# Performance work log

Hardware: AMD Instinct MI355X
Metric: run time of the kernel (lower is better)

The kernel has to match this reference:

```python
import jax, jax.numpy as jnp
import numpy as np

B, T, E, H, L = 16, 512, 768, 12, 100
D = E // H
LN_EPS = 1e-12
NEG = -1e9


def setup_inputs() -> dict:
    key = jax.random.key(0)
    ks = jax.random.split(key, 12)
    s = 1.0 / np.sqrt(E)
    inp = {
        "last_hidden_states": jax.random.normal(ks[0], (B, T, E), jnp.float32),
        "att_mask": jnp.ones((B, T), jnp.float32),
        "type_emb": jax.random.normal(ks[1], (L, E), jnp.float32),
        # learned params
        "tp": jax.random.normal(ks[2], (E,), jnp.float32),
        "Wq": jax.random.normal(ks[3], (E, E), jnp.float32) * s,
        "bq": jnp.zeros((E,), jnp.float32),
        "Wk": jax.random.normal(ks[4], (E, E), jnp.float32) * s,
        "bk": jnp.zeros((E,), jnp.float32),
        "Wv": jax.random.normal(ks[5], (E, E), jnp.float32) * s,
        "bv": jnp.zeros((E,), jnp.float32),
        "Wo": jax.random.normal(ks[6], (E, E), jnp.float32) * s,
        "bo": jnp.zeros((E,), jnp.float32),
        "ln_g": jnp.ones((E,), jnp.float32),
        "ln_b": jnp.zeros((E,), jnp.float32),
    }
    return inp


def _layer_norm(x, g, b):
    mu = x.mean(-1, keepdims=True)
    var = ((x - mu) ** 2).mean(-1, keepdims=True)
    return (x - mu) * jax.lax.rsqrt(var + LN_EPS) * g + b


def reference(last_hidden_states, att_mask, type_emb, tp,
              Wq, bq, Wk, bk, Wv, bv, Wo, bo, ln_g, ln_b):
    b, t, e = last_hidden_states.shape
    # --- label cross-attention (no head split, no scaling) ---
    scores = jnp.einsum('bte,le->btl', last_hidden_states, type_emb)      # [b,t,l]
    att = jax.nn.softmax(scores, axis=-1)
    first_label_emb = jnp.einsum('btl,le->bte', att, type_emb)            # [b,t,e]

    h_truth = last_hidden_states + first_label_emb
    h_unknown = last_hidden_states + tp                                   # broadcast tp over [b,t]

    # --- two-stream masked self-attention: Q from unknown, K/V from truth,
    #     each position masked from attending to its own truth state ---
    q = (h_unknown @ Wq + bq).reshape(b, t, H, D)
    k = (h_truth @ Wk + bk).reshape(b, t, H, D)
    v = (h_truth @ Wv + bv).reshape(b, t, H, D)
    logits = jnp.einsum('bqhd,bkhd->bhqk', q, k) / np.sqrt(D).astype(np.float32)
    pad_bias = (1.0 - att_mask)[:, None, None, :] * NEG                   # [b,1,1,t]
    diag_bias = jnp.eye(t, dtype=logits.dtype)[None, None] * NEG          # [1,1,t,t]
    probs = jax.nn.softmax(logits + pad_bias + diag_bias, axis=-1)
    ctx = jnp.einsum('bhqk,bkhd->bqhd', probs, v).reshape(b, t, e)
    attn_out = ctx @ Wo + bo
    twice_hidden = _layer_norm(attn_out + h_unknown, ln_g, ln_b)

    out = twice_hidden + last_hidden_states + first_label_emb
    return out, scores
```

## Files before the change

kernel.cpp:

```cpp
#include <hip/hip_runtime.h>

typedef unsigned char u8;
typedef unsigned short u16;
typedef u16 u16x4 __attribute__((ext_vector_type(4)));
typedef u16 u16x8 __attribute__((ext_vector_type(8)));
typedef __bf16 bf16x8 __attribute__((ext_vector_type(8)));
typedef float f32x2 __attribute__((ext_vector_type(2)));
typedef float f32x4 __attribute__((ext_vector_type(4)));
typedef long longx2 __attribute__((ext_vector_type(2)));

#define BB 16
#define TT 512
#define EE 768
#define HH 12
#define DD 64
#define LL 100
#define BT (BB*TT)
#define BTE ((size_t)BT*EE)
#define LOG2E 1.44269504f
#define QSCALE (0.125f*LOG2E)
#define FIXMAX 44.0f

__device__ __forceinline__ float bf2f(u16 u){
  union { float f; unsigned int i; } v; v.i = ((unsigned int)u) << 16; return v.f;
}
__device__ __forceinline__ u16 f2bf(float f){
  __bf16 h = (__bf16)f;
  union { __bf16 h; u16 u; } v; v.h = h; return v.u;
}
__device__ __forceinline__ u16 pk_fp8(float a, float b){
  return (u16)(__builtin_amdgcn_cvt_pk_fp8_f32(a, b, 0, false) & 0xffff);
}
__device__ __forceinline__ u8 f2fp8(float a){
  return (u8)(__builtin_amdgcn_cvt_pk_fp8_f32(a, 0.f, 0, false) & 0xff);
}

__device__ __forceinline__ void gload16(const void* g, void* l){
  __builtin_amdgcn_global_load_lds(
      (const __attribute__((address_space(1))) void*)g,
      (__attribute__((address_space(3))) void*)l, 16, 0, 0);
}

__global__ __launch_bounds__(256,1) void prep_all_kernel(
    const float* __restrict__ Wq, const float* __restrict__ Wk,
    const float* __restrict__ Wv, const float* __restrict__ Wo,
    u8* __restrict__ WT8,
    const float* __restrict__ TE, u16* __restrict__ TEb, u16* __restrict__ TEt,
    const float* __restrict__ mask, float* __restrict__ MBg)
{
  __shared__ float tile[64][65];
  int bx = blockIdx.x;
  int tid = threadIdx.x;
  if (bx < 576){
    int m  = bx / 144, t = bx % 144;
    int tr = t / 12,  tc = t % 12;
    const float* W = (m==0)?Wq : (m==1)?Wk : (m==2)?Wv : Wo;
    u8* dst = WT8 + (size_t)m * EE * EE;
#pragma unroll
    for (int i=0;i<16;i++){
      int idx = tid + 256*i; int r = idx>>6, c = idx&63;
      tile[r][c] = W[(size_t)(tr*64+r)*EE + tc*64 + c];
    }
    __syncthreads();
#pragma unroll
    for (int i=0;i<8;i++){
      int idx = tid + 256*i;
      int r = idx >> 5, cp = idx & 31;
      u16 pk = pk_fp8(tile[cp*2][r], tile[cp*2+1][r]);
      *(u16*)&dst[(size_t)(tc*64+r)*EE + tr*64 + cp*2] = pk;
    }
  } else if (bx < 960){
    int e = (bx - 576)*2 + (tid >> 7);
    int c = tid & 127;
    u16 v = 0;
    if (c < LL) v = f2bf(TE[(size_t)c*EE + e]);
    TEt[(size_t)e*128 + c] = v;
    if (e < 128){
#pragma unroll
      for (int k=c; k<EE; k+=128)
        TEb[(size_t)e*EE + k] = (e < LL) ? f2bf(TE[(size_t)e*EE + k]) : (u16)0;
    }
  } else {
    int i = (bx - 960)*256 + tid;
    MBg[i] = (1.0f - mask[i]) * (-1e9f * LOG2E) - FIXMAX;
  }
}

__global__ __launch_bounds__(64) void label_scores_kernel(
    const float* __restrict__ X, const u16* __restrict__ TEb,
    float* __restrict__ scores_out, u16* __restrict__ att)
{
  int m0 = blockIdx.x * 16;
  int lane = threadIdx.x;
  int l15 = lane & 15, g = lane >> 4;

  const float* xrow = X + (size_t)(m0 + l15)*EE;
  f32x4 s[7] = {};
  for (int k0=0; k0<EE; k0+=64){
    bf16x8 af[2];
#pragma unroll
    for (int kk=0;kk<2;kk++){
      const float* src = xrow + k0 + kk*32 + g*8;
      float4 a = *(const float4*)src, b = *(const float4*)(src+4);
      bf16x8 o;
      o[0]=(__bf16)a.x; o[1]=(__bf16)a.y; o[2]=(__bf16)a.z; o[3]=(__bf16)a.w;
      o[4]=(__bf16)b.x; o[5]=(__bf16)b.y; o[6]=(__bf16)b.z; o[7]=(__bf16)b.w;
      af[kk] = o;
    }
#pragma unroll
    for (int nt=0;nt<7;nt++){
      bf16x8 b0 = *(const bf16x8*)&TEb[(size_t)(nt*16+l15)*EE + k0 + g*8];
      bf16x8 b1 = *(const bf16x8*)&TEb[(size_t)(nt*16+l15)*EE + k0 + 32 + g*8];
      s[nt] = __builtin_amdgcn_mfma_f32_16x16x32_bf16(af[0], b0, s[nt], 0,0,0);
      s[nt] = __builtin_amdgcn_mfma_f32_16x16x32_bf16(af[1], b1, s[nt], 0,0,0);
    }
  }

  int rowb = m0 + g*4;
#pragma unroll
  for (int nt=0;nt<7;nt++){
    int col = nt*16 + l15;
    if (col < LL){
#pragma unroll
      for (int r=0;r<4;r++)
        scores_out[(size_t)(rowb + r)*LL + col] = s[nt][r];
    }
  }
  if (l15 >= 4){
#pragma unroll
    for (int r=0;r<4;r++) s[6][r] = -1e30f;
  }
  float inv[4];
#pragma unroll
  for (int r=0;r<4;r++){
    float tm = s[0][r];
#pragma unroll
    for (int nt=1;nt<7;nt++) tm = fmaxf(tm, s[nt][r]);
    tm = fmaxf(tm, __shfl_xor(tm, 1, 16));
    tm = fmaxf(tm, __shfl_xor(tm, 2, 16));
    tm = fmaxf(tm, __shfl_xor(tm, 4, 16));
    tm = fmaxf(tm, __shfl_xor(tm, 8, 16));
    float ps = 0.f;
#pragma unroll
    for (int nt=0;nt<7;nt++){
      float p = exp2f((s[nt][r] - tm) * LOG2E);
      s[nt][r] = p; ps += p;
    }
    ps += __shfl_xor(ps, 1, 16);
    ps += __shfl_xor(ps, 2, 16);
    ps += __shfl_xor(ps, 4, 16);
    ps += __shfl_xor(ps, 8, 16);
    inv[r] = 1.f/ps;
  }
#pragma unroll
  for (int nt=0;nt<7;nt++){
    int col = nt*16 + l15;
#pragma unroll
    for (int r=0;r<4;r++)
      att[(size_t)(rowb + r)*128 + col] = f2bf(s[nt][r] * inv[r]);
  }
  {
    int col = 112 + l15;
#pragma unroll
    for (int r=0;r<4;r++) att[(size_t)(rowb + r)*128 + col] = 0;
  }
}

__global__ __launch_bounds__(256,1) void gemm_fle_kernel(
    const u16* __restrict__ A, const u16* __restrict__ BTw,
    const float* __restrict__ Xf, const float* __restrict__ tp,
    u8* __restrict__ HT8, u8* __restrict__ HU8, int N, int K)
{
  __shared__ u16 As[128*40];
  __shared__ u16 Bs[128*40];
  int nb = N >> 7;
  int m0 = (blockIdx.x / nb) << 7;
  int n0 = (blockIdx.x % nb) << 7;
  int tid  = threadIdx.x, lane = tid & 63, w = tid >> 6;
  int wm = (w >> 1) << 6, wn = (w & 1) << 6;
  int lr = lane & 15, lk = (lane >> 4) << 3;

  f32x4 acc[4][4] = {};

  for (int k0 = 0; k0 < K; k0 += 32){
    __syncthreads();
#pragma unroll
    for (int i=0;i<2;i++){
      int idx = tid + (i<<8);
      int row = idx >> 2, kq = (idx & 3) << 3;
      *(u16x8*)&As[row*40 + kq] = *(const u16x8*)&A  [(size_t)(m0+row)*K + k0 + kq];
      *(u16x8*)&Bs[row*40 + kq] = *(const u16x8*)&BTw[(size_t)(n0+row)*K + k0 + kq];
    }
    __syncthreads();
    bf16x8 af[4], bfr[4];
#pragma unroll
    for (int i=0;i<4;i++) af [i] = *(const bf16x8*)&As[(wm + i*16 + lr)*40 + lk];
#pragma unroll
    for (int j=0;j<4;j++) bfr[j] = *(const bf16x8*)&Bs[(wn + j*16 + lr)*40 + lk];
#pragma unroll
    for (int i=0;i<4;i++)
#pragma unroll
      for (int j=0;j<4;j++)
        acc[i][j] = __builtin_amdgcn_mfma_f32_16x16x32_bf16(af[i], bfr[j], acc[i][j], 0, 0, 0);
  }

  int rbase = (lane >> 4) << 2;
#pragma unroll
  for (int j=0;j<4;j++){
    int col = n0 + wn + j*16 + lr;
    float tpv = tp[col];
#pragma unroll
    for (int i=0;i<4;i++){
#pragma unroll
      for (int r=0;r<4;r++){
        int row = m0 + wm + i*16 + rbase + r;
        float x = Xf[(size_t)row*EE + col];
        HT8[(size_t)row*EE + col] = f2fp8(x + acc[i][j][r]);
        HU8[(size_t)row*EE + col] = f2fp8(x + tpv);
      }
    }
  }
}

template<int NB, int FUSED>
__global__ __launch_bounds__(256,2) void gemm8_kernel(
    const u8* __restrict__ A0, const u8* __restrict__ A1,
    const u8* __restrict__ Wb,
    const float* __restrict__ b0, const float* __restrict__ b1,
    const float* __restrict__ b2,
    u16* __restrict__ C0, u16* __restrict__ C1, u16* __restrict__ C2)
{
  __shared__ __align__(16) u8 As[128*128];
  __shared__ __align__(16) u8 Bs[128*128];
  const int K = EE;

  int nwg = gridDim.x;
  int bid = blockIdx.x;
  int cpx = nwg >> 3;
  int swz = (bid & 7) * cpx + (bid >> 3);
  int mb = swz / NB, nb = swz % NB;
  int m0 = mb << 7;
  int n0 = (FUSED ? (nb % 6) : nb) << 7;

  int which = FUSED ? (nb / 6) : 0;
  const u8* Ap; const u8* Wp; const float* bp; u16* Cp;
  if (!FUSED){ Ap = A0; Wp = Wb; bp = b0; Cp = C0; }
  else {
    if (which == 0){ Ap = A0; Wp = Wb;                      bp = b0; Cp = C0; }
    else if (which == 1){ Ap = A1; Wp = Wb + (size_t)EE*EE; bp = b1; Cp = C1; }
    else { Ap = A1; Wp = Wb + 2*(size_t)EE*EE;              bp = b2; Cp = C2; }
  }

  int tid = threadIdx.x, lane = tid & 63, w = tid >> 6;
  int wm = (w >> 1) << 6, wn = (w & 1) << 6;
  int lr = lane & 15, g = lane >> 4;
  int lrow = lane >> 3;
  int lchunk = (lane & 7) ^ lrow;

  f32x4 acc[4][4] = {};

  for (int k0 = 0; k0 < K; k0 += 128){
    __syncthreads();
#pragma unroll
    for (int t=0;t<4;t++){
      int r0 = w*32 + t*8;
      gload16(&Ap[(size_t)(m0 + r0 + lrow)*K + k0 + (lchunk<<4)], &As[r0*128]);
      gload16(&Wp[(size_t)(n0 + r0 + lrow)*K + k0 + (lchunk<<4)], &Bs[r0*128]);
    }
    __syncthreads();
#pragma unroll
    for (int t=0;t<2;t++){
      int cs = ((t<<2) + g) ^ (lr & 7);
      longx2 af[4], bfr[4];
#pragma unroll
      for (int i=0;i<4;i++) af [i] = *(const longx2*)&As[(wm + i*16 + lr)*128 + (cs<<4)];
#pragma unroll
      for (int j=0;j<4;j++) bfr[j] = *(const longx2*)&Bs[(wn + j*16 + lr)*128 + (cs<<4)];
#pragma unroll
      for (int i=0;i<4;i++)
#pragma unroll
        for (int j=0;j<4;j++){
          acc[i][j] = __builtin_amdgcn_mfma_f32_16x16x32_fp8_fp8(af[i][0], bfr[j][0], acc[i][j], 0, 0, 0);
          acc[i][j] = __builtin_amdgcn_mfma_f32_16x16x32_fp8_fp8(af[i][1], bfr[j][1], acc[i][j], 0, 0, 0);
        }
    }
  }

  int rbase = (lane >> 4) << 2;
  float scq = (FUSED && which==0) ? QSCALE : 1.0f;
#pragma unroll
  for (int j=0;j<4;j++){
    int col = n0 + wn + j*16 + lr;
    float bv = bp[col];
    if (FUSED && which == 2){
      int hh = col >> 6, d = col & 63;
#pragma unroll
      for (int i=0;i<4;i++){
        int row0 = m0 + wm + i*16 + rbase;
        int bb = row0 >> 9, t0 = row0 & 511;
        u16x4 o;
#pragma unroll
        for (int r=0;r<4;r++) o[r] = f2bf(acc[i][j][r] + bv);
        *(u16x4*)&Cp[((size_t)(bb*HH + hh)*DD + d)*TT + t0] = o;
      }
    } else {
#pragma unroll
      for (int i=0;i<4;i++){
#pragma unroll
        for (int r=0;r<4;r++){
          int row = m0 + wm + i*16 + rbase + r;
          Cp[(size_t)row*EE + col] = f2bf((acc[i][j][r] + bv) * scq);
        }
      }
    }
  }
}

__global__ __launch_bounds__(256,3) void attn_mfma_kernel(
    const u16* __restrict__ Q, const u16* __restrict__ K,
    const u16* __restrict__ VT, const float* __restrict__ MBg,
    u8* __restrict__ CTX8)
{
  __shared__ u16 Ks [2][64*64];
  __shared__ u16 VTs[2][64*64];
  __shared__ u16 Pl [4][32*72];

  int bx = blockIdx.x;
  int bh = bx % (BB*HH), q0 = (bx / (BB*HH)) << 7;
  int b = bh / HH, h = bh % HH;
  int tid = threadIdx.x, lane = tid & 63, w = tid >> 6;
  int l15 = lane & 15, g = lane >> 4;
  int wq0 = q0 + w*32;
  size_t rowbase = (size_t)b*TT;
  u16* pw = &Pl[w][0];
  const u16* Kbh = K  + rowbase*EE + h*DD;
  const u16* Vbh = VT + (size_t)bh*DD*TT;
  int lrow = lane >> 3, lchunk = (lane & 7) ^ (lane >> 3);

  bf16x8 qf[2][2];
#pragma unroll
  for (int i=0;i<2;i++)
#pragma unroll
    for (int kk=0;kk<2;kk++)
      qf[i][kk] = *(const bf16x8*)&Q[(rowbase + wq0 + i*16 + l15)*EE + h*DD + kk*32 + g*8];

  f32x4 ctxf[2][4] = {};
  float lrun[2][4] = {};

#define STAGE(buf, k0)                                                          \
  { _Pragma("unroll")                                                           \
    for (int it=0; it<2; ++it){                                                 \
      int r0 = w*16 + it*8;                                                     \
      gload16(&Kbh[(size_t)((k0) + r0 + lrow)*EE + (lchunk<<3)], &Ks [buf][r0*64]); \
      gload16(&Vbh[(size_t)(r0 + lrow)*TT + (k0) + (lchunk<<3)], &VTs[buf][r0*64]); } }

  STAGE(0, 0);

  for (int kt=0; kt<8; ++kt){
    int k0 = kt << 6;
    int buf = kt & 1;
    __syncthreads();

    float mb[4];
#pragma unroll
    for (int kb=0;kb<4;kb++) mb[kb] = MBg[rowbase + k0 + kb*16 + l15];

    if (kt < 7) STAGE(buf^1, k0+64);

    f32x4 s[2][4] = {};
#pragma unroll
    for (int kk=0;kk<2;kk++){
      int cs = ((kk<<2) + g) ^ (l15 & 7);
      bf16x8 kf[4];
#pragma unroll
      for (int kb=0;kb<4;kb++)
        kf[kb] = *(const bf16x8*)&Ks[buf][(kb*16 + l15)*64 + (cs<<3)];
#pragma unroll
      for (int i=0;i<2;i++)
#pragma unroll
        for (int kb=0;kb<4;kb++)
          s[i][kb] = __builtin_amdgcn_mfma_f32_16x16x32_bf16(qf[i][kk], kf[kb], s[i][kb], 0,0,0);
    }

    if ((k0 < wq0 + 32) && (k0 + 64 > wq0)){
#pragma unroll
      for (int i=0;i<2;i++){
        int qr = wq0 + i*16 + g*4;
#pragma unroll
        for (int kb=0;kb<4;kb++){
          int kpos = k0 + kb*16 + l15;
#pragma unroll
          for (int r=0;r<4;r++)
            if (kpos == qr + r) s[i][kb][r] -= 1e9f*LOG2E;
        }
      }
    }

#pragma unroll
    for (int i=0;i<2;i++)
#pragma unroll
      for (int kb=0;kb<4;kb++)
#pragma unroll
        for (int r=0;r<4;r++){
          float p = exp2f(s[i][kb][r] + mb[kb]);
          lrun[i][r] += p;
          pw[(i*16 + g*4 + r)*72 + kb*16 + l15] = f2bf(p);
        }

    bf16x8 pa[2][2];
#pragma unroll
    for (int i=0;i<2;i++)
#pragma unroll
      for (int kk=0;kk<2;kk++)
        pa[i][kk] = *(const bf16x8*)&pw[(i*16 + l15)*72 + kk*32 + g*8];

#pragma unroll
    for (int kk=0;kk<2;kk++){
      int cs = ((kk<<2) + g) ^ (l15 & 7);
      bf16x8 vf[4];
#pragma unroll
      for (int dj=0;dj<4;dj++)
        vf[dj] = *(const bf16x8*)&VTs[buf][(dj*16 + l15)*64 + (cs<<3)];
#pragma unroll
      for (int i=0;i<2;i++)
#pragma unroll
        for (int dj=0;dj<4;dj++)
          ctxf[i][dj] = __builtin_amdgcn_mfma_f32_16x16x32_bf16(pa[i][kk], vf[dj], ctxf[i][dj], 0,0,0);
    }
  }
#undef STAGE

  float inv[2][4];
#pragma unroll
  for (int i=0;i<2;i++)
#pragma unroll
    for (int r=0;r<4;r++){
      float l = lrun[i][r];
      l += __shfl_xor(l, 1, 16);
      l += __shfl_xor(l, 2, 16);
      l += __shfl_xor(l, 4, 16);
      l += __shfl_xor(l, 8, 16);
      inv[i][r] = 1.0f / l;
    }
#pragma unroll
  for (int i=0;i<2;i++)
#pragma unroll
    for (int dj=0;dj<4;dj++)
#pragma unroll
      for (int r=0;r<4;r++)
        pw[(i*16 + g*4 + r)*64 + dj*16 + l15] = f2bf(ctxf[i][dj][r] * inv[i][r]);
#pragma unroll
  for (int t=0;t<4;t++){
    int row = lane >> 1, c = ((lane & 1)<<5) + t*8;
    const u16* pv = &pw[row*64 + c];
    u16x4 o8;
#pragma unroll
    for (int e=0;e<4;e++) o8[e] = pk_fp8(bf2f(pv[2*e]), bf2f(pv[2*e+1]));
    *(u16x4*)&CTX8[(rowbase + wq0 + row)*EE + h*DD + c] = o8;
  }
}

__global__ __launch_bounds__(192,1) void ln_out_kernel(
    const u16* __restrict__ AO, const u8* __restrict__ HU8,
    const u8* __restrict__ HT8, const float* __restrict__ g,
    const float* __restrict__ bta, float* __restrict__ out)
{
  __shared__ float red[3];
  int r = blockIdx.x, tid = threadIdx.x;
  size_t base = (size_t)r*EE;
  int e0 = tid*4;
  u16x4 ao = *(const u16x4*)&AO[base+e0];
  int hu4 = *(const int*)&HU8[base+e0];
  int ht4 = *(const int*)&HT8[base+e0];
  f32x2 hulo = __builtin_amdgcn_cvt_pk_f32_fp8(hu4, false);
  f32x2 huhi = __builtin_amdgcn_cvt_pk_f32_fp8(hu4, true);
  f32x2 htlo = __builtin_amdgcn_cvt_pk_f32_fp8(ht4, false);
  f32x2 hthi = __builtin_amdgcn_cvt_pk_f32_fp8(ht4, true);
  float huv[4] = {hulo[0], hulo[1], huhi[0], huhi[1]};
  float htv[4] = {htlo[0], htlo[1], hthi[0], hthi[1]};
  float x[4];
#pragma unroll
  for (int j=0;j<4;j++) x[j] = bf2f(ao[j]) + huv[j];

  float s = x[0]+x[1]+x[2]+x[3];
#pragma unroll
  for (int o=32;o;o>>=1) s += __shfl_xor(s, o, 64);
  int w = tid>>6;
  if ((tid&63)==0) red[w] = s;
  __syncthreads();
  float mu = (red[0]+red[1]+red[2]) * (1.0f/EE);
  __syncthreads();
  float d2 = 0.f;
#pragma unroll
  for (int j=0;j<4;j++){ float d = x[j]-mu; d2 += d*d; }
#pragma unroll
  for (int o=32;o;o>>=1) d2 += __shfl_xor(d2, o, 64);
  if ((tid&63)==0) red[w] = d2;
  __syncthreads();
  float var = (red[0]+red[1]+red[2]) * (1.0f/EE);
  float rs = rsqrtf(var + 1e-12f);
  float4 gg = *(const float4*)&g[e0];
  float4 bb = *(const float4*)&bta[e0];
  float4 o4;
  o4.x = (x[0]-mu)*rs*gg.x + bb.x + htv[0];
  o4.y = (x[1]-mu)*rs*gg.y + bb.y + htv[1];
  o4.z = (x[2]-mu)*rs*gg.z + bb.z + htv[2];
  o4.w = (x[3]-mu)*rs*gg.w + bb.w + htv[3];
  *(float4*)&out[base+e0] = o4;
}

extern "C" void kernel_launch(void* const* d_in, const int* in_sizes, int n_in,
                              void* d_out, int out_size, void* d_ws, size_t ws_size,
                              hipStream_t stream)
{
  (void)in_sizes; (void)n_in; (void)out_size; (void)ws_size;
  const float* X    = (const float*)d_in[0];
  const float* mask = (const float*)d_in[1];
  const float* TE   = (const float*)d_in[2];
  const float* tp   = (const float*)d_in[3];
  const float* Wq   = (const float*)d_in[4];
  const float* bq   = (const float*)d_in[5];
  const float* Wk   = (const float*)d_in[6];
  const float* bk   = (const float*)d_in[7];
  const float* Wv   = (const float*)d_in[8];
  const float* bv   = (const float*)d_in[9];
  const float* Wo   = (const float*)d_in[10];
  const float* bo   = (const float*)d_in[11];
  const float* ln_g = (const float*)d_in[12];
  const float* ln_b = (const float*)d_in[13];

  float* out    = (float*)d_out;
  float* scores = out + BTE;

  char* p = (char*)d_ws;
  u8*  HT8  = (u8*)p;  p += BTE;
  u8*  HU8  = (u8*)p;  p += BTE;
  u8*  CTX8 = (u8*)p;  p += BTE;
  u8*  WT8  = (u8*)p;  p += (size_t)4*EE*EE;
  u16* Qb   = (u16*)p; p += BTE*2;
  u16* Kb   = (u16*)p; p += BTE*2;
  u16* VTb  = (u16*)p; p += BTE*2;
  u16* AOb  = (u16*)p; p += BTE*2;
  u16* ATT  = (u16*)p; p += (size_t)BT*128*2;
  u16* TEb  = (u16*)p; p += (size_t)128*EE*2;
  u16* TEt  = (u16*)p; p += (size_t)EE*128*2;
  float* MBg = (float*)p;

  prep_all_kernel<<<dim3(992), dim3(256), 0, stream>>>(
      Wq, Wk, Wv, Wo, WT8, TE, TEb, TEt, mask, MBg);

  label_scores_kernel<<<dim3(BT/16), dim3(64), 0, stream>>>(X, TEb, scores, ATT);

  gemm_fle_kernel<<<dim3((BT/128)*(EE/128)), dim3(256), 0, stream>>>(
      ATT, TEt, X, tp, HT8, HU8, EE, 128);

  gemm8_kernel<18,1><<<dim3(64*18), dim3(256), 0, stream>>>(
      HU8, HT8, WT8, bq, bk, bv, Qb, Kb, VTb);

  attn_mfma_kernel<<<dim3(BB*HH*4), dim3(256), 0, stream>>>(Qb, Kb, VTb, MBg, CTX8);

  gemm8_kernel<6,0><<<dim3(64*6), dim3(256), 0, stream>>>(
      CTX8, nullptr, WT8 + 3*(size_t)EE*EE, bo, nullptr, nullptr, AOb, nullptr, nullptr);

  ln_out_kernel<<<dim3(BT), dim3(192), 0, stream>>>(AOb, HU8, HT8, ln_g, ln_b, out);
}
```

Measured before the change: 116.2 us.

## Double-buffer LDS tiles in fp8 GEMM to overlap global loads with MFMA

The fp8 projection GEMM now keeps two LDS buffers for its A and B tiles. It prefetches the next K-slice while MFMAs run on the current one, and uses explicit vmcnt waits plus barriers in place of the two __syncthreads per iteration. The goal is to hide global-to-LDS load latency behind compute. LDS use doubles to 64KB per block, which may limit the two-blocks-per-CU occupancy target, and correctness now depends on the hand-written waitcnt counts.

```diff
diff --git a/kernel.cpp b/kernel.cpp
--- a/kernel.cpp
+++ b/kernel.cpp
@@ -230,8 +230,8 @@
     const float* __restrict__ b2,
     u16* __restrict__ C0, u16* __restrict__ C1, u16* __restrict__ C2)
 {
-  __shared__ __align__(16) u8 As[128*128];
-  __shared__ __align__(16) u8 Bs[128*128];
+  __shared__ __align__(16) u8 As[2][128*128];
+  __shared__ __align__(16) u8 Bs[2][128*128];
   const int K = EE;
 
   int nwg = gridDim.x;
@@ -259,23 +259,31 @@
 
   f32x4 acc[4][4] = {};
 
-  for (int k0 = 0; k0 < K; k0 += 128){
-    __syncthreads();
-#pragma unroll
-    for (int t=0;t<4;t++){
-      int r0 = w*32 + t*8;
-      gload16(&Ap[(size_t)(m0 + r0 + lrow)*K + k0 + (lchunk<<4)], &As[r0*128]);
-      gload16(&Wp[(size_t)(n0 + r0 + lrow)*K + k0 + (lchunk<<4)], &Bs[r0*128]);
-    }
-    __syncthreads();
+#define GST(buf, k0)                                                            \
+  { _Pragma("unroll")                                                           \
+    for (int t=0;t<4;t++){                                                      \
+      int r0 = w*32 + t*8;                                                      \
+      gload16(&Ap[(size_t)(m0 + r0 + lrow)*K + (k0) + (lchunk<<4)], &As[buf][r0*128]); \
+      gload16(&Wp[(size_t)(n0 + r0 + lrow)*K + (k0) + (lchunk<<4)], &Bs[buf][r0*128]); } }
+
+  GST(0, 0);
+  GST(1, 128);
+
+#pragma unroll
+  for (int ks = 0; ks < 6; ks++){
+    int buf = ks & 1;
+    if (ks == 5) { asm volatile("s_waitcnt vmcnt(0)" ::: "memory"); }
+    else         { asm volatile("s_waitcnt vmcnt(8)" ::: "memory"); }
+    __builtin_amdgcn_sched_barrier(0);
+    __builtin_amdgcn_s_barrier();
 #pragma unroll
     for (int t=0;t<2;t++){
       int cs = ((t<<2) + g) ^ (lr & 7);
       longx2 af[4], bfr[4];
 #pragma unroll
-      for (int i=0;i<4;i++) af [i] = *(const longx2*)&As[(wm + i*16 + lr)*128 + (cs<<4)];
-#pragma unroll
-      for (int j=0;j<4;j++) bfr[j] = *(const longx2*)&Bs[(wn + j*16 + lr)*128 + (cs<<4)];
+      for (int i=0;i<4;i++) af [i] = *(const longx2*)&As[buf][(wm + i*16 + lr)*128 + (cs<<4)];
+#pragma unroll
+      for (int j=0;j<4;j++) bfr[j] = *(const longx2*)&Bs[buf][(wn + j*16 + lr)*128 + (cs<<4)];
 #pragma unroll
       for (int i=0;i<4;i++)
 #pragma unroll
@@ -284,7 +292,10 @@
           acc[i][j] = __builtin_amdgcn_mfma_f32_16x16x32_fp8_fp8(af[i][1], bfr[j][1], acc[i][j], 0, 0, 0);
         }
     }
-  }
+    __builtin_amdgcn_s_barrier();
+    if (ks < 4) GST(buf, (ks << 7) + 256);
+  }
+#undef GST
 
   int rbase = (lane >> 4) << 2;
   float scq = (FUSED && which==0) ? QSCALE : 1.0f;
```

New measurement: 120.0 us. 3.3% more time.
